# Performance work log

Measured on AMD Instinct MI355X. Metric: run time of the kernel, lower is better.

## Reference

```python
import jax, jax.numpy as jnp
import numpy as np

B, S, H, N, NREL = 16, 2048, 1024, 128, 8


def setup_inputs() -> dict:
    key = jax.random.key(0)
    ks = jax.random.split(key, 8)
    word_emb = jax.random.normal(ks[0], (B, S, H), dtype=jnp.float32)
    num_ids = jax.random.randint(ks[1], (B, N), 0, S)  # all valid (no -1 padding)
    is_response = jax.random.randint(ks[2], (B, N), 0, 2).astype(jnp.int32)
    numbers = jax.random.normal(ks[3], (B, N), dtype=jnp.float32)
    scale = 1.0 / np.sqrt(H).astype(np.float32)
    w_alpha = jax.random.normal(ks[4], (H, 1), dtype=jnp.float32) * scale
    b_alpha = jnp.zeros((1,), dtype=jnp.float32)
    w_f = jax.random.normal(ks[5], (H, H), dtype=jnp.float32) * scale
    b_f = jnp.zeros((H,), dtype=jnp.float32)
    W_r = jax.random.normal(ks[6], (NREL, H, H), dtype=jnp.float32) * scale  # 8 bias-free relation linears
    return dict(word_emb=word_emb, num_ids=num_ids, is_response=is_response,
                numbers=numbers, w_alpha=w_alpha, b_alpha=b_alpha,
                w_f=w_f, b_f=b_f, W_r=W_r)


def reference(word_emb, num_ids, is_response, numbers, w_alpha, b_alpha, w_f, b_f, W_r):
    Bn, Sn, Hn = word_emb.shape
    Nn = num_ids.shape[1]
    mask = (num_ids >= 0)  # [B,N] valid-node mask (original uses -1 padding)
    idx = jnp.clip(num_ids, 0, Sn - 1)
    # per-batch gather: Init[b,n] = word_emb[b, num_ids[b,n]]  -> [B,N,H]
    Init = jnp.take_along_axis(word_emb, idx[:, :, None], axis=1)
    alpha = jax.nn.sigmoid(Init @ w_alpha + b_alpha)  # [B,N,1]
    # all 8 relation transforms of every sender node j: T[b,r,j,:] = Init[b,j] @ W_r[r].T
    T = jnp.einsum('bnh,rkh->brnk', Init, W_r)  # [B,8,N,H]
    # relation id r(b,i,j) = 4*(num_i>num_j) + 2*resp_i + resp_j
    gt = (numbers[:, :, None] > numbers[:, None, :]).astype(jnp.int32)  # [B,N,N]
    resp = (is_response == 1).astype(jnp.int32)
    R = 4 * gt + 2 * resp[:, :, None] + resp[:, None, :]  # [B,N,N]
    sel = jax.nn.one_hot(R, NREL, dtype=word_emb.dtype)  # [B,N,N,8]
    not_diag = ~jnp.eye(Nn, dtype=bool)
    # edge weight over sender j: alpha_j, valid i & j, i != j
    wgt = (alpha[:, None, :, 0] * mask[:, None, :] * mask[:, :, None]
           * not_diag[None]).astype(word_emb.dtype)  # [B,N,N]
    Temp = jnp.einsum('bijr,brjh->bih', sel * wgt[..., None], T)  # [B,N,H]
    n_nodes = mask.sum(axis=1)  # [B]
    denom = jnp.maximum(n_nodes - 1, 1).astype(word_emb.dtype)
    Temp = Temp / denom[:, None, None]
    out = jax.nn.relu(Init @ w_f + b_f + Temp)  # [B,N,H]
    return out
```

## Files before the change

kernel.cpp:

```cpp
#include <hip/hip_runtime.h>
#include <hip/hip_bf16.h>
#include <stdint.h>

#define B_ 16
#define S_ 2048
#define H_ 1024
#define N_ 128
#define M_ (B_*N_)
#define K5 5120
#define MP 2176

typedef __attribute__((ext_vector_type(8))) short s8vec;
typedef __attribute__((ext_vector_type(4))) float f4vec;
typedef __hip_bfloat16 bf16;

__global__ void k_sort(const int* __restrict__ num_ids, const int* __restrict__ is_resp,
                       const float* __restrict__ numbers,
                       int* __restrict__ sigma, int* __restrict__ newgrp,
                       int* __restrict__ respv, float* __restrict__ denom) {
    int b = blockIdx.x, i = threadIdx.x;
    __shared__ float nums[N_];
    __shared__ int sig[N_];
    __shared__ int cnt;
    float ni = numbers[b*N_ + i];
    int idv = num_ids[b*N_ + i];
    int valid = (idv >= 0) ? 1 : 0;
    nums[i] = ni;
    if (i == 0) cnt = 0;
    __syncthreads();
    int p = 0;
    for (int j = 0; j < N_; ++j) {
        float nj = nums[j];
        p += (nj < ni || (nj == ni && j < i)) ? 1 : 0;
    }
    sig[p] = i;
    atomicAdd(&cnt, valid);
    __syncthreads();
    sigma[b*N_ + i] = sig[i];
    int cur = sig[i];
    int prv = (i > 0) ? sig[i-1] : 0;
    newgrp[b*N_ + i] = (i == 0 || nums[cur] != nums[prv]) ? 1 : 0;
    respv[b*N_ + i] = ((is_resp[b*N_ + i] == 1) ? 1 : 0) | (valid << 1);
    if (i == 0) denom[b] = fmaxf((float)(cnt - 1), 1.0f);
}

__global__ void k_meta(const int* __restrict__ respv, int* __restrict__ aperm,
                       int* __restrict__ iperm, int* __restrict__ meta) {
    __shared__ int s0[1024], s1[1024];
    int t = threadIdx.x;
    aperm[t] = -1; aperm[t + 1024] = -1;
    if (t < MP - 2048) aperm[t + 2048] = -1;
    int r0 = 2*t, r1 = 2*t + 1;
    int c_a = respv[r0] & 1, c_b = respv[r1] & 1;
    int a0 = 1 - c_a, b0 = 1 - c_b;
    s0[t] = a0 + b0;
    s1[t] = c_a + c_b;
    __syncthreads();
    for (int off = 1; off < 1024; off <<= 1) {
        int v0 = (t >= off) ? s0[t-off] : 0;
        int v1 = (t >= off) ? s1[t-off] : 0;
        __syncthreads();
        s0[t] += v0; s1[t] += v1;
        __syncthreads();
    }
    int C0 = s0[1023], C1 = s1[1023];
    int P0 = ((C0 + 127) >> 7) << 7;
    int ex0 = s0[t] - (a0 + b0);
    int ex1 = s1[t] - (c_a + c_b);
    int p_a = (c_a == 0) ? ex0 : P0 + ex1;
    int p_b = (c_b == 0) ? ex0 + a0 : P0 + ex1 + c_a;
    aperm[p_a] = r0; iperm[r0] = p_a;
    aperm[p_b] = r1; iperm[r1] = p_b;
    if (t == 0) { meta[0] = P0; meta[1] = C0; meta[2] = C1; }
}

__global__ void k_gather(const float* __restrict__ word_emb, const int* __restrict__ num_ids,
                         const float* __restrict__ w_alpha, const float* __restrict__ b_alpha,
                         const float* __restrict__ denom, const int* __restrict__ iperm,
                         bf16* __restrict__ A, float* __restrict__ ascaled) {
    int blk = blockIdx.x;
    int b = blk >> 7, n = blk & 127;
    int t = threadIdx.x;
    int idv = num_ids[b*N_ + n];
    int valid = (idv >= 0) ? 1 : 0;
    int idx = idv < 0 ? 0 : (idv > S_-1 ? S_-1 : idv);
    int pr = iperm[b*N_ + n];
    const float4* row = (const float4*)(word_emb + ((size_t)b*S_ + idx)*H_);
    float4 v = row[t];
    float4 w = ((const float4*)w_alpha)[t];
    float part = v.x*w.x + v.y*w.y + v.z*w.z + v.w*w.w;
    bf16* dst = A + (size_t)pr*K5 + 4*H_ + t*4;
    dst[0] = __float2bfloat16(v.x);
    dst[1] = __float2bfloat16(v.y);
    dst[2] = __float2bfloat16(v.z);
    dst[3] = __float2bfloat16(v.w);
#pragma unroll
    for (int off = 32; off > 0; off >>= 1) part += __shfl_down(part, off, 64);
    __shared__ float red[4];
    if ((t & 63) == 0) red[t >> 6] = part;
    __syncthreads();
    if (t == 0) {
        float dot = red[0] + red[1] + red[2] + red[3] + b_alpha[0];
        float al = 1.0f / (1.0f + __expf(-dot));
        ascaled[b*N_ + n] = valid ? (al / denom[b]) : 0.0f;
    }
}

__global__ void k_wt(const float* __restrict__ W_r, bf16* __restrict__ Wt) {
    size_t o = ((size_t)blockIdx.x*256 + threadIdx.x)*4;
    int cs = (int)(o >> 20);
    int c = cs >> 2, s = cs & 3;
    int r = ((s >> 1) << 2) + 2*c + (s & 1);
    size_t off = o & (size_t)(H_*H_ - 1);
    float4 v = *(const float4*)(W_r + (size_t)r*H_*H_ + off);
    bf16* dst = Wt + (size_t)(c*5 + s)*H_*H_ + off;
    dst[0] = __float2bfloat16(v.x);
    dst[1] = __float2bfloat16(v.y);
    dst[2] = __float2bfloat16(v.z);
    dst[3] = __float2bfloat16(v.w);
}

__global__ void k_wf(const float* __restrict__ w_f, bf16* __restrict__ Wt) {
    __shared__ float lds[64][65];
    int bi = blockIdx.x, bj = blockIdx.y;
    int t = threadIdx.x;
    int ty = t >> 4, tx = t & 15;
#pragma unroll
    for (int i = 0; i < 4; ++i) {
        int r = ty*4 + i;
        float4 v = *(const float4*)(w_f + (size_t)(bi*64 + r)*H_ + bj*64 + tx*4);
        lds[r][tx*4+0] = v.x; lds[r][tx*4+1] = v.y;
        lds[r][tx*4+2] = v.z; lds[r][tx*4+3] = v.w;
    }
    __syncthreads();
    bf16* d0 = Wt + (size_t)4*H_*H_;
    bf16* d1 = Wt + (size_t)9*H_*H_;
#pragma unroll
    for (int i = 0; i < 4; ++i) {
        int n = ty*4 + i;
        size_t doff = (size_t)(bj*64 + n)*H_ + bi*64 + tx*4;
#pragma unroll
        for (int j = 0; j < 4; ++j) {
            bf16 val = __float2bfloat16(lds[tx*4+j][n]);
            d0[doff + j] = val;
            d1[doff + j] = val;
        }
    }
}

__global__ void k_pad(const int* __restrict__ aperm, bf16* __restrict__ A) {
    int pr = blockIdx.x;
    if (aperm[pr] >= 0) return;
    float4 z = {0.f, 0.f, 0.f, 0.f};
    float4* dst = (float4*)(A + (size_t)pr*K5);
    for (int c = threadIdx.x; c < 640; c += 256) dst[c] = z;
}

__global__ void k_build(const float* __restrict__ ascaled, const int* __restrict__ sigma,
                        const int* __restrict__ newgrp, const int* __restrict__ respv,
                        const int* __restrict__ iperm, bf16* __restrict__ A) {
    int b = blockIdx.y;
    int h = blockIdx.x*64 + threadIdx.x;
    __shared__ float as_s[N_];
    __shared__ int sig_s[N_], ng_s[N_], rv_s[N_], pm_s[N_];
    for (int j = threadIdx.x; j < N_; j += 64) {
        as_s[j] = ascaled[b*N_ + j];
        sig_s[j] = sigma[b*N_ + j];
        ng_s[j] = newgrp[b*N_ + j];
        rv_s[j] = respv[b*N_ + j];
        pm_s[j] = iperm[b*N_ + j];
    }
    __syncthreads();
    const bf16* initcol = A + 4*H_ + h;
    float tot0 = 0.f, tot1 = 0.f;
    for (int i2 = 0; i2 < N_; ++i2) {
        float v = as_s[i2] * __bfloat162float(initcol[(size_t)pm_s[i2]*K5]);
        if (rv_s[i2] & 1) tot1 += v; else tot0 += v;
    }
    float cS0=0.f, cS1=0.f, cG0=0.f, cG1=0.f;
    for (int p = 0; p < N_; ++p) {
        int i2 = sig_s[p];
        if (ng_s[p]) { cS0 += cG0; cS1 += cG1; cG0 = 0.f; cG1 = 0.f; }
        float v = as_s[i2] * __bfloat162float(initcol[(size_t)pm_s[i2]*K5]);
        int resp = rv_s[i2] & 1;
        float vf = (rv_s[i2] >> 1) ? 1.0f : 0.0f;
        float G0 = cS0, G1 = cS1;
        float L0 = tot0 - G0 - (resp ? 0.f : v);
        float L1 = tot1 - G1 - (resp ? v : 0.f);
        bf16* Ar = A + (size_t)pm_s[i2]*K5 + h;
        Ar[0*H_] = __float2bfloat16(L0*vf);
        Ar[1*H_] = __float2bfloat16(L1*vf);
        Ar[2*H_] = __float2bfloat16(G0*vf);
        Ar[3*H_] = __float2bfloat16(G1*vf);
        if (resp) cG1 += v; else cG0 += v;
    }
}

#define BM 128
#define BN 128
#define BK 32

__global__ __launch_bounds__(256) void k_gemm(const bf16* __restrict__ A,
                                              const bf16* __restrict__ Wt,
                                              const int* __restrict__ meta,
                                              float* __restrict__ acc_buf) {
    __shared__ __align__(16) bf16 As[BM*BK];
    __shared__ __align__(16) bf16 Bs[BN*BK];
    int tid = threadIdx.x;
    int w = tid >> 6, lane = tid & 63;
    int q = lane >> 4, r = lane & 15;
    int bid = blockIdx.x;
    int mt = bid % 17;
    int rest = bid / 17;
    int nt = rest & 7, ks = rest >> 3;
    int rowBase = mt * BM, colBase = nt * BN;
    int wm = w >> 1, wn = w & 1;
    int P0 = meta[0];
    const bf16* Wtc = Wt + ((rowBase >= P0) ? (size_t)5*H_*H_ : 0) + (size_t)ks*H_*H_;

    f4vec acc[4][4];
#pragma unroll
    for (int mi = 0; mi < 4; ++mi)
#pragma unroll
        for (int ni = 0; ni < 4; ++ni)
#pragma unroll
            for (int e = 0; e < 4; ++e) acc[mi][ni][e] = 0.0f;

    const size_t Abase = (size_t)rowBase * K5 + (size_t)ks * H_;
    const int swz = q ^ ((r >> 2) & 3);

    for (int kin = 0; kin < 1024; kin += BK) {
        {
            int c = tid;
            int p = (c & 3) ^ ((c >> 4) & 3);
            const bf16* g = A + Abase + (size_t)(c >> 2)*K5 + kin + p*8;
            __builtin_amdgcn_global_load_lds((const __attribute__((address_space(1))) void*)g,
                (__attribute__((address_space(3))) void*)((char*)As + w*1024), 16, 0, 0);
            c = tid + 256;
            p = (c & 3) ^ ((c >> 4) & 3);
            const bf16* g2 = A + Abase + (size_t)(c >> 2)*K5 + kin + p*8;
            __builtin_amdgcn_global_load_lds((const __attribute__((address_space(1))) void*)g2,
                (__attribute__((address_space(3))) void*)((char*)As + 4096 + w*1024), 16, 0, 0);
            c = tid;
            p = (c & 3) ^ ((c >> 4) & 3);
            const bf16* gb = Wtc + (size_t)(colBase + (c >> 2))*H_ + kin + p*8;
            __builtin_amdgcn_global_load_lds((const __attribute__((address_space(1))) void*)gb,
                (__attribute__((address_space(3))) void*)((char*)Bs + w*1024), 16, 0, 0);
            c = tid + 256;
            p = (c & 3) ^ ((c >> 4) & 3);
            const bf16* gb2 = Wtc + (size_t)(colBase + (c >> 2))*H_ + kin + p*8;
            __builtin_amdgcn_global_load_lds((const __attribute__((address_space(1))) void*)gb2,
                (__attribute__((address_space(3))) void*)((char*)Bs + 4096 + w*1024), 16, 0, 0);
        }
        __syncthreads();
        const short* Asp = (const short*)As;
        const short* Bsp = (const short*)Bs;
        s8vec af[4], bfr[4];
#pragma unroll
        for (int mi = 0; mi < 4; ++mi) {
            int R = wm*64 + mi*16 + r;
            af[mi] = *(const s8vec*)(Asp + R*32 + (swz << 3));
        }
#pragma unroll
        for (int ni = 0; ni < 4; ++ni) {
            int C = wn*64 + ni*16 + r;
            bfr[ni] = *(const s8vec*)(Bsp + C*32 + (swz << 3));
        }
#pragma unroll
        for (int mi = 0; mi < 4; ++mi)
#pragma unroll
            for (int ni = 0; ni < 4; ++ni)
                acc[mi][ni] = __builtin_amdgcn_mfma_f32_16x16x32_bf16(af[mi], bfr[ni],
                                                                      acc[mi][ni], 0, 0, 0);
        __syncthreads();
    }

#pragma unroll
    for (int mi = 0; mi < 4; ++mi)
#pragma unroll
        for (int ni = 0; ni < 4; ++ni)
#pragma unroll
            for (int e = 0; e < 4; ++e) {
                int rr = rowBase + wm*64 + mi*16 + q*4 + e;
                int cc = colBase + wn*64 + ni*16 + r;
                atomicAdd(&acc_buf[(size_t)rr*H_ + cc], acc[mi][ni][e]);
            }
}

__global__ void k_epi(const float* __restrict__ acc_buf, const int* __restrict__ iperm,
                      const float* __restrict__ b_f, float* __restrict__ out) {
    int row = blockIdx.x;
    int pr = iperm[row];
    int t = threadIdx.x;
    float4 v = ((const float4*)(acc_buf + (size_t)pr*H_))[t];
    float4 bv = ((const float4*)b_f)[t];
    v.x = fmaxf(v.x + bv.x, 0.0f);
    v.y = fmaxf(v.y + bv.y, 0.0f);
    v.z = fmaxf(v.z + bv.z, 0.0f);
    v.w = fmaxf(v.w + bv.w, 0.0f);
    ((float4*)(out + (size_t)row*H_))[t] = v;
}

extern "C" void kernel_launch(void* const* d_in, const int* in_sizes, int n_in,
                              void* d_out, int out_size, void* d_ws, size_t ws_size,
                              hipStream_t stream) {
    (void)in_sizes; (void)n_in; (void)out_size; (void)ws_size;
    const float* word_emb = (const float*)d_in[0];
    const int*   num_ids  = (const int*)d_in[1];
    const int*   is_resp  = (const int*)d_in[2];
    const float* numbers  = (const float*)d_in[3];
    const float* w_alpha  = (const float*)d_in[4];
    const float* b_alpha  = (const float*)d_in[5];
    const float* w_f      = (const float*)d_in[6];
    const float* b_f      = (const float*)d_in[7];
    const float* W_r      = (const float*)d_in[8];
    float* out = (float*)d_out;

    char* ws = (char*)d_ws;
    bf16*  Aws     = (bf16*)(ws);
    bf16*  Wt      = (bf16*)(ws + 22282240);
    float* acc_buf = (float*)(ws + 43253760);
    float* ascaled = (float*)(ws + 52166656);
    int*   sigma   = (int*)(ws + 52174848);
    int*   newgrp  = (int*)(ws + 52183040);
    int*   respv   = (int*)(ws + 52191232);
    float* denom   = (float*)(ws + 52199424);
    int*   aperm   = (int*)(ws + 52199488);
    int*   iperm   = (int*)(ws + 52208192);
    int*   meta    = (int*)(ws + 52216384);

    hipMemsetAsync(acc_buf, 0, (size_t)MP*H_*sizeof(float), stream);
    k_sort  <<<16,   128, 0, stream>>>(num_ids, is_resp, numbers, sigma, newgrp, respv, denom);
    k_meta  <<<1,   1024, 0, stream>>>(respv, aperm, iperm, meta);
    k_gather<<<2048, 256, 0, stream>>>(word_emb, num_ids, w_alpha, b_alpha, denom, iperm,
                                       Aws, ascaled);
    k_wt    <<<8192, 256, 0, stream>>>(W_r, Wt);
    k_wf    <<<dim3(16,16), 256, 0, stream>>>(w_f, Wt);
    k_pad   <<<MP,   256, 0, stream>>>(aperm, Aws);
    k_build <<<dim3(16,16), 64, 0, stream>>>(ascaled, sigma, newgrp, respv, iperm, Aws);
    k_gemm  <<<680,  256, 0, stream>>>(Aws, Wt, meta, acc_buf);
    k_epi   <<<2048, 256, 0, stream>>>(acc_buf, iperm, b_f, out);
}
```

Before: 348.7 us.

## Drop split-K atomics, fuse bias-ReLU epilogue into double-buffered GEMM

```diff
diff --git a/kernel.cpp b/kernel.cpp
--- a/kernel.cpp
+++ b/kernel.cpp
@@ -11,6 +11,7 @@
 #define MP 2176
 
 typedef __attribute__((ext_vector_type(8))) short s8vec;
+typedef __attribute__((ext_vector_type(4))) short s4vec;
 typedef __attribute__((ext_vector_type(4))) float f4vec;
 typedef __hip_bfloat16 bf16;
 
@@ -89,11 +90,12 @@
     float4 v = row[t];
     float4 w = ((const float4*)w_alpha)[t];
     float part = v.x*w.x + v.y*w.y + v.z*w.z + v.w*w.w;
-    bf16* dst = A + (size_t)pr*K5 + 4*H_ + t*4;
-    dst[0] = __float2bfloat16(v.x);
-    dst[1] = __float2bfloat16(v.y);
-    dst[2] = __float2bfloat16(v.z);
-    dst[3] = __float2bfloat16(v.w);
+    union { s4vec v4; bf16 h[4]; } pk;
+    pk.h[0] = __float2bfloat16(v.x);
+    pk.h[1] = __float2bfloat16(v.y);
+    pk.h[2] = __float2bfloat16(v.z);
+    pk.h[3] = __float2bfloat16(v.w);
+    *(s4vec*)(A + (size_t)pr*K5 + 4*H_ + t*4) = pk.v4;
 #pragma unroll
     for (int off = 32; off > 0; off >>= 1) part += __shfl_down(part, off, 64);
     __shared__ float red[4];
@@ -107,17 +109,19 @@
 }
 
 __global__ void k_wt(const float* __restrict__ W_r, bf16* __restrict__ Wt) {
-    size_t o = ((size_t)blockIdx.x*256 + threadIdx.x)*4;
+    size_t o = ((size_t)blockIdx.x*256 + threadIdx.x)*8;
     int cs = (int)(o >> 20);
     int c = cs >> 2, s = cs & 3;
     int r = ((s >> 1) << 2) + 2*c + (s & 1);
     size_t off = o & (size_t)(H_*H_ - 1);
-    float4 v = *(const float4*)(W_r + (size_t)r*H_*H_ + off);
-    bf16* dst = Wt + (size_t)(c*5 + s)*H_*H_ + off;
-    dst[0] = __float2bfloat16(v.x);
-    dst[1] = __float2bfloat16(v.y);
-    dst[2] = __float2bfloat16(v.z);
-    dst[3] = __float2bfloat16(v.w);
+    const float4* src = (const float4*)(W_r + (size_t)r*H_*H_ + off);
+    float4 v0 = src[0], v1 = src[1];
+    union { s8vec v8; bf16 h[8]; } pk;
+    pk.h[0] = __float2bfloat16(v0.x); pk.h[1] = __float2bfloat16(v0.y);
+    pk.h[2] = __float2bfloat16(v0.z); pk.h[3] = __float2bfloat16(v0.w);
+    pk.h[4] = __float2bfloat16(v1.x); pk.h[5] = __float2bfloat16(v1.y);
+    pk.h[6] = __float2bfloat16(v1.z); pk.h[7] = __float2bfloat16(v1.w);
+    *(s8vec*)(Wt + (size_t)(c*5 + s)*H_*H_ + off) = pk.v8;
 }
 
 __global__ void k_wf(const float* __restrict__ w_f, bf16* __restrict__ Wt) {
@@ -139,21 +143,12 @@
     for (int i = 0; i < 4; ++i) {
         int n = ty*4 + i;
         size_t doff = (size_t)(bj*64 + n)*H_ + bi*64 + tx*4;
-#pragma unroll
-        for (int j = 0; j < 4; ++j) {
-            bf16 val = __float2bfloat16(lds[tx*4+j][n]);
-            d0[doff + j] = val;
-            d1[doff + j] = val;
-        }
-    }
-}
-
-__global__ void k_pad(const int* __restrict__ aperm, bf16* __restrict__ A) {
-    int pr = blockIdx.x;
-    if (aperm[pr] >= 0) return;
-    float4 z = {0.f, 0.f, 0.f, 0.f};
-    float4* dst = (float4*)(A + (size_t)pr*K5);
-    for (int c = threadIdx.x; c < 640; c += 256) dst[c] = z;
+        union { s4vec v4; bf16 h[4]; } pk;
+#pragma unroll
+        for (int j = 0; j < 4; ++j) pk.h[j] = __float2bfloat16(lds[tx*4+j][n]);
+        *(s4vec*)(d0 + doff) = pk.v4;
+        *(s4vec*)(d1 + doff) = pk.v4;
+    }
 }
 
 __global__ void k_build(const float* __restrict__ ascaled, const int* __restrict__ sigma,
@@ -198,25 +193,27 @@
 
 #define BM 128
 #define BN 128
-#define BK 32
+#define BK 64
+#define NSTEP (K5/BK)
 
 __global__ __launch_bounds__(256) void k_gemm(const bf16* __restrict__ A,
                                               const bf16* __restrict__ Wt,
                                               const int* __restrict__ meta,
-                                              float* __restrict__ acc_buf) {
-    __shared__ __align__(16) bf16 As[BM*BK];
-    __shared__ __align__(16) bf16 Bs[BN*BK];
+                                              const int* __restrict__ aperm,
+                                              const float* __restrict__ b_f,
+                                              float* __restrict__ out) {
+    __shared__ __align__(16) bf16 As0[BM*BK], As1[BM*BK];
+    __shared__ __align__(16) bf16 Bs0[BN*BK], Bs1[BN*BK];
     int tid = threadIdx.x;
     int w = tid >> 6, lane = tid & 63;
     int q = lane >> 4, r = lane & 15;
     int bid = blockIdx.x;
-    int mt = bid % 17;
-    int rest = bid / 17;
-    int nt = rest & 7, ks = rest >> 3;
+    int wg = (bid & 7)*17 + (bid >> 3);
+    int mt = wg % 17, nt = wg / 17;
     int rowBase = mt * BM, colBase = nt * BN;
     int wm = w >> 1, wn = w & 1;
     int P0 = meta[0];
-    const bf16* Wtc = Wt + ((rowBase >= P0) ? (size_t)5*H_*H_ : 0) + (size_t)ks*H_*H_;
+    const bf16* Wtc = Wt + ((rowBase >= P0) ? (size_t)5*H_*H_ : 0);
 
     f4vec acc[4][4];
 #pragma unroll
@@ -226,79 +223,73 @@
 #pragma unroll
             for (int e = 0; e < 4; ++e) acc[mi][ni][e] = 0.0f;
 
-    const size_t Abase = (size_t)rowBase * K5 + (size_t)ks * H_;
-    const int swz = q ^ ((r >> 2) & 3);
-
-    for (int kin = 0; kin < 1024; kin += BK) {
-        {
-            int c = tid;
-            int p = (c & 3) ^ ((c >> 4) & 3);
-            const bf16* g = A + Abase + (size_t)(c >> 2)*K5 + kin + p*8;
-            __builtin_amdgcn_global_load_lds((const __attribute__((address_space(1))) void*)g,
-                (__attribute__((address_space(3))) void*)((char*)As + w*1024), 16, 0, 0);
-            c = tid + 256;
-            p = (c & 3) ^ ((c >> 4) & 3);
-            const bf16* g2 = A + Abase + (size_t)(c >> 2)*K5 + kin + p*8;
-            __builtin_amdgcn_global_load_lds((const __attribute__((address_space(1))) void*)g2,
-                (__attribute__((address_space(3))) void*)((char*)As + 4096 + w*1024), 16, 0, 0);
-            c = tid;
-            p = (c & 3) ^ ((c >> 4) & 3);
-            const bf16* gb = Wtc + (size_t)(colBase + (c >> 2))*H_ + kin + p*8;
+    auto STAGE = [&](bf16* AsB, bf16* BsB, int kin) {
+        int slot = kin >> 10, koff = kin & 1023;
+        const bf16* Wslot = Wtc + ((size_t)slot << 20);
+#pragma unroll
+        for (int j = 0; j < 4; ++j) {
+            int c = tid + j*256;
+            int row = c >> 3;
+            int p = (c & 7) ^ (row & 7);
+            const bf16* ga = A + (size_t)(rowBase + row)*K5 + kin + p*8;
+            __builtin_amdgcn_global_load_lds((const __attribute__((address_space(1))) void*)ga,
+                (__attribute__((address_space(3))) void*)((char*)AsB + j*4096 + w*1024), 16, 0, 0);
+            const bf16* gb = Wslot + ((size_t)(colBase + row) << 10) + koff + p*8;
             __builtin_amdgcn_global_load_lds((const __attribute__((address_space(1))) void*)gb,
-                (__attribute__((address_space(3))) void*)((char*)Bs + w*1024), 16, 0, 0);
-            c = tid + 256;
-            p = (c & 3) ^ ((c >> 4) & 3);
-            const bf16* gb2 = Wtc + (size_t)(colBase + (c >> 2))*H_ + kin + p*8;
-            __builtin_amdgcn_global_load_lds((const __attribute__((address_space(1))) void*)gb2,
-                (__attribute__((address_space(3))) void*)((char*)Bs + 4096 + w*1024), 16, 0, 0);
+                (__attribute__((address_space(3))) void*)((char*)BsB + j*4096 + w*1024), 16, 0, 0);
         }
+    };
+
+    auto COMPUTE = [&](const bf16* AsB, const bf16* BsB) {
+        const short* Asp = (const short*)AsB;
+        const short* Bsp = (const short*)BsB;
+        s8vec af[2][4], bfr[2][4];
+#pragma unroll
+        for (int kk = 0; kk < 2; ++kk) {
+            int sl = ((kk*4 + q) ^ (r & 7)) << 3;
+#pragma unroll
+            for (int mi = 0; mi < 4; ++mi)
+                af[kk][mi] = *(const s8vec*)(Asp + (wm*64 + mi*16 + r)*BK + sl);
+#pragma unroll
+            for (int ni = 0; ni < 4; ++ni)
+                bfr[kk][ni] = *(const s8vec*)(Bsp + (wn*64 + ni*16 + r)*BK + sl);
+        }
+#pragma unroll
+        for (int kk = 0; kk < 2; ++kk)
+#pragma unroll
+            for (int mi = 0; mi < 4; ++mi)
+#pragma unroll
+                for (int ni = 0; ni < 4; ++ni)
+                    acc[mi][ni] = __builtin_amdgcn_mfma_f32_16x16x32_bf16(
+                        af[kk][mi], bfr[kk][ni], acc[mi][ni], 0, 0, 0);
+    };
+
+    STAGE(As0, Bs0, 0);
+    for (int t = 0; t < NSTEP; t += 2) {
         __syncthreads();
-        const short* Asp = (const short*)As;
-        const short* Bsp = (const short*)Bs;
-        s8vec af[4], bfr[4];
-#pragma unroll
-        for (int mi = 0; mi < 4; ++mi) {
-            int R = wm*64 + mi*16 + r;
-            af[mi] = *(const s8vec*)(Asp + R*32 + (swz << 3));
+        if (t + 1 < NSTEP) STAGE(As1, Bs1, (t+1)*BK);
+        COMPUTE(As0, Bs0);
+        __syncthreads();
+        if (t + 2 < NSTEP) STAGE(As0, Bs0, (t+2)*BK);
+        COMPUTE(As1, Bs1);
+    }
+
+    float bias[4];
+#pragma unroll
+    for (int ni = 0; ni < 4; ++ni) bias[ni] = b_f[colBase + wn*64 + ni*16 + r];
+#pragma unroll
+    for (int mi = 0; mi < 4; ++mi) {
+        int rb = rowBase + wm*64 + mi*16 + q*4;
+        int og0 = aperm[rb+0], og1 = aperm[rb+1], og2 = aperm[rb+2], og3 = aperm[rb+3];
+#pragma unroll
+        for (int ni = 0; ni < 4; ++ni) {
+            int cc = colBase + wn*64 + ni*16 + r;
+            if (og0 >= 0) out[(size_t)og0*H_ + cc] = fmaxf(acc[mi][ni][0] + bias[ni], 0.0f);
+            if (og1 >= 0) out[(size_t)og1*H_ + cc] = fmaxf(acc[mi][ni][1] + bias[ni], 0.0f);
+            if (og2 >= 0) out[(size_t)og2*H_ + cc] = fmaxf(acc[mi][ni][2] + bias[ni], 0.0f);
+            if (og3 >= 0) out[(size_t)og3*H_ + cc] = fmaxf(acc[mi][ni][3] + bias[ni], 0.0f);
         }
-#pragma unroll
-        for (int ni = 0; ni < 4; ++ni) {
-            int C = wn*64 + ni*16 + r;
-            bfr[ni] = *(const s8vec*)(Bsp + C*32 + (swz << 3));
-        }
-#pragma unroll
-        for (int mi = 0; mi < 4; ++mi)
-#pragma unroll
-            for (int ni = 0; ni < 4; ++ni)
-                acc[mi][ni] = __builtin_amdgcn_mfma_f32_16x16x32_bf16(af[mi], bfr[ni],
-                                                                      acc[mi][ni], 0, 0, 0);
-        __syncthreads();
-    }
-
-#pragma unroll
-    for (int mi = 0; mi < 4; ++mi)
-#pragma unroll
-        for (int ni = 0; ni < 4; ++ni)
-#pragma unroll
-            for (int e = 0; e < 4; ++e) {
-                int rr = rowBase + wm*64 + mi*16 + q*4 + e;
-                int cc = colBase + wn*64 + ni*16 + r;
-                atomicAdd(&acc_buf[(size_t)rr*H_ + cc], acc[mi][ni][e]);
-            }
-}
-
-__global__ void k_epi(const float* __restrict__ acc_buf, const int* __restrict__ iperm,
-                      const float* __restrict__ b_f, float* __restrict__ out) {
-    int row = blockIdx.x;
-    int pr = iperm[row];
-    int t = threadIdx.x;
-    float4 v = ((const float4*)(acc_buf + (size_t)pr*H_))[t];
-    float4 bv = ((const float4*)b_f)[t];
-    v.x = fmaxf(v.x + bv.x, 0.0f);
-    v.y = fmaxf(v.y + bv.y, 0.0f);
-    v.z = fmaxf(v.z + bv.z, 0.0f);
-    v.w = fmaxf(v.w + bv.w, 0.0f);
-    ((float4*)(out + (size_t)row*H_))[t] = v;
+    }
 }
 
 extern "C" void kernel_launch(void* const* d_in, const int* in_sizes, int n_in,
@@ -319,7 +310,6 @@
     char* ws = (char*)d_ws;
     bf16*  Aws     = (bf16*)(ws);
     bf16*  Wt      = (bf16*)(ws + 22282240);
-    float* acc_buf = (float*)(ws + 43253760);
     float* ascaled = (float*)(ws + 52166656);
     int*   sigma   = (int*)(ws + 52174848);
     int*   newgrp  = (int*)(ws + 52183040);
@@ -329,15 +319,12 @@
     int*   iperm   = (int*)(ws + 52208192);
     int*   meta    = (int*)(ws + 52216384);
 
-    hipMemsetAsync(acc_buf, 0, (size_t)MP*H_*sizeof(float), stream);
     k_sort  <<<16,   128, 0, stream>>>(num_ids, is_resp, numbers, sigma, newgrp, respv, denom);
     k_meta  <<<1,   1024, 0, stream>>>(respv, aperm, iperm, meta);
     k_gather<<<2048, 256, 0, stream>>>(word_emb, num_ids, w_alpha, b_alpha, denom, iperm,
                                        Aws, ascaled);
-    k_wt    <<<8192, 256, 0, stream>>>(W_r, Wt);
+    k_wt    <<<4096, 256, 0, stream>>>(W_r, Wt);
     k_wf    <<<dim3(16,16), 256, 0, stream>>>(w_f, Wt);
-    k_pad   <<<MP,   256, 0, stream>>>(aperm, Aws);
     k_build <<<dim3(16,16), 64, 0, stream>>>(ascaled, sigma, newgrp, respv, iperm, Aws);
-    k_gemm  <<<680,  256, 0, stream>>>(Aws, Wt, meta, acc_buf);
-    k_epi   <<<2048, 256, 0, stream>>>(acc_buf, iperm, b_f, out);
-}
+    k_gemm  <<<136,  256, 0, stream>>>(Aws, Wt, meta, aperm, b_f, out);
+}
```

Result: no change. 346.3 us (-0.7%).
